# Kernel tuning notes

Measured on AMD Instinct MI355X. Metric: run time of the kernel, lower is better.

Reference implementation:

```python
import jax, jax.numpy as jnp
import numpy as np
from jax import lax

VOCAB = 32000
EMB = 1024
HID = 1024
SEQ = 128
BATCH = 32
FORGET_BIAS = 1.0


def setup_inputs() -> dict:
    key = jax.random.key(0)
    ks = jax.random.split(key, 8)
    u = lambda k, shape: jax.random.uniform(k, shape, jnp.float32, -0.1, 0.1)
    inp = {
        'input_seq': jax.random.randint(ks[0], (SEQ, BATCH), 0, VOCAB, dtype=jnp.int64),
        'emb': u(ks[1], (VOCAB, EMB)),
        # BasicLSTMCell kernel: [(input_dim + hidden), 4*hidden], bias [4*hidden]
        'W0': u(ks[2], (EMB + HID, 4 * HID)),
        'b0': jnp.zeros((4 * HID,), jnp.float32),
        'W1': u(ks[3], (HID + HID, 4 * HID)),
        'b1': jnp.zeros((4 * HID,), jnp.float32),
        'Wd': u(ks[4], (HID, VOCAB)),
        'bd': jnp.zeros((VOCAB,), jnp.float32),
    }
    return inp


def _lstm_layer(x_seq, W, b):
    """Static unrolled BasicLSTMCell as a lax.scan. x_seq: [T, B, D]."""
    T, B, _ = x_seq.shape
    H = b.shape[0] // 4

    def step(carry, x):
        c, h = carry
        z = jnp.concatenate([x, h], axis=-1) @ W + b  # [B, 4H]
        i, j, f, o = jnp.split(z, 4, axis=-1)  # gate order of BasicLSTMCell
        c2 = c * jax.nn.sigmoid(f + FORGET_BIAS) + jax.nn.sigmoid(i) * jnp.tanh(j)
        h2 = jnp.tanh(c2) * jax.nn.sigmoid(o)
        return (c2, h2), h2

    init = (jnp.zeros((B, H), x_seq.dtype), jnp.zeros((B, H), x_seq.dtype))
    _, ys = lax.scan(step, init, x_seq)
    return ys  # [T, B, H]


def reference(input_seq, emb, W0, b0, W1, b1, Wd, bd):
    y = emb[input_seq]                      # [T, B, EMB] embedding lookup
    y = _lstm_layer(y, W0, b0)              # layer 1
    y = _lstm_layer(y, W1, b1)              # layer 2
    logits = y.reshape(-1, y.shape[-1]) @ Wd + bd  # [T*B, VOCAB]
    return logits
```

## Files before the change

kernel.cpp:

```cpp
#include <hip/hip_runtime.h>

#define VOCAB 32000
#define EMB   1024
#define HID   1024
#define SEQ   128
#define BATCH 32
#define ROWS  (SEQ * BATCH)
#define G4    (4 * HID)
#define SSEG  512
#define SSLOT 65536

typedef __bf16 bf16x8 __attribute__((ext_vector_type(8)));
typedef float  f32x4  __attribute__((ext_vector_type(4)));

__device__ __forceinline__ unsigned short f2bf(float f) {
  union { float f; unsigned int u; } v; v.f = f;
  unsigned int r = v.u + 0x7fffu + ((v.u >> 16) & 1u);
  return (unsigned short)(r >> 16);
}
__device__ __forceinline__ float bf2f(unsigned short u) {
  union { unsigned int u; float f; } v; v.u = ((unsigned int)u) << 16;
  return v.f;
}

__device__ __forceinline__ void async16(const void* g, void* l) {
  __builtin_amdgcn_global_load_lds(
      (const __attribute__((address_space(1))) void*)g,
      (__attribute__((address_space(3))) void*)l, 16, 0, 0);
}

__device__ __forceinline__ float fsigmoid(float x) {
  return __builtin_amdgcn_rcpf(1.f + __expf(-x));
}
__device__ __forceinline__ float ftanh(float x) {
  return 1.f - 2.f * __builtin_amdgcn_rcpf(__expf(2.f * x) + 1.f);
}

__global__ void embed_split(const int* __restrict__ ids, const float* __restrict__ emb,
                            unsigned short* __restrict__ Xp) {
  int r = blockIdx.x;
  int t = r >> 5, b = r & 31;
  int row = ids[r];
  int e = threadIdx.x * 4;
  const float4 v = *reinterpret_cast<const float4*>(emb + (size_t)row * EMB + e);
  ushort4 hi, lo;
  hi.x = f2bf(v.x); lo.x = f2bf(v.x - bf2f(hi.x));
  hi.y = f2bf(v.y); lo.y = f2bf(v.y - bf2f(hi.y));
  hi.z = f2bf(v.z); lo.z = f2bf(v.z - bf2f(hi.z));
  hi.w = f2bf(v.w); lo.w = f2bf(v.w - bf2f(hi.w));
  unsigned short* dst = Xp + (size_t)t * SSLOT + (e >> 3) * SSEG + b * 16 + (e & 7);
  *reinterpret_cast<ushort4*>(dst)     = hi;
  *reinterpret_cast<ushort4*>(dst + 8) = lo;
}

__global__ void wsplit_kernel(const float* __restrict__ in, unsigned short* __restrict__ hi,
                              unsigned short* __restrict__ lo, int K, int N) {
  __shared__ float t[32][33];
  int n0 = blockIdx.x * 32, k0 = blockIdx.y * 32;
  int tx = threadIdx.x, ty = threadIdx.y;
#pragma unroll
  for (int i = 0; i < 4; ++i)
    t[ty + i * 8][tx] = in[(size_t)(k0 + ty + i * 8) * N + n0 + tx];
  __syncthreads();
#pragma unroll
  for (int i = 0; i < 4; ++i) {
    float v = t[tx][ty + i * 8];
    unsigned short h = f2bf(v);
    hi[(size_t)(n0 + ty + i * 8) * K + k0 + tx] = h;
    lo[(size_t)(n0 + ty + i * 8) * K + k0 + tx] = f2bf(v - bf2f(h));
  }
}

__global__ void transpose_kernel(const float* __restrict__ in, unsigned short* __restrict__ out,
                                 int K, int N) {
  __shared__ float t[32][33];
  int n0 = blockIdx.x * 32, k0 = blockIdx.y * 32;
  int tx = threadIdx.x, ty = threadIdx.y;
#pragma unroll
  for (int i = 0; i < 4; ++i)
    t[ty + i * 8][tx] = in[(size_t)(k0 + ty + i * 8) * N + n0 + tx];
  __syncthreads();
#pragma unroll
  for (int i = 0; i < 4; ++i)
    out[(size_t)(n0 + ty + i * 8) * K + k0 + tx] = f2bf(t[tx][ty + i * 8]);
}

__global__ __launch_bounds__(512, 2) void lstm_ring(
    const unsigned short* __restrict__ Xp,
    const unsigned short* __restrict__ W0hi, const unsigned short* __restrict__ W0lo,
    const unsigned short* __restrict__ W1hi, const unsigned short* __restrict__ W1lo,
    const float* __restrict__ b0, const float* __restrict__ b1,
    unsigned short* __restrict__ H2,
    unsigned short* h1r, unsigned short* h2r,
    unsigned int* F0, unsigned int* F1)
{
  __shared__ float zl[8][32][36];

  const int tid   = threadIdx.x;
  const int lane  = tid & 63;
  const int w     = tid >> 6;
  const int layer = blockIdx.x >> 7;
  const int wg    = blockIdx.x & 127;
  const int j0    = wg * 8;
  const int lrow  = lane & 15;
  const int klo   = (lane >> 4) * 8;

  const unsigned short* Whi = layer ? W1hi : W0hi;
  const unsigned short* Wlo = layer ? W1lo : W0lo;
  const float*          bias = layer ? b1 : b0;

  bf16x8 wh[2][8], wl[2][8];
#pragma unroll
  for (int nt = 0; nt < 2; ++nt) {
    int n = nt * 16 + lrow;
    size_t grow = (size_t)((n >> 3) * 1024 + j0 + (n & 7));
    const unsigned short* bh = Whi + grow * 2048 + w * 256 + klo;
    const unsigned short* bl = Wlo + grow * 2048 + w * 256 + klo;
#pragma unroll
    for (int ks = 0; ks < 8; ++ks) {
      wh[nt][ks] = *reinterpret_cast<const bf16x8*>(bh + ks * 32);
      wl[nt][ks] = *reinterpret_cast<const bf16x8*>(bl + ks * 32);
    }
  }

  const int eb = tid >> 3;
  const int ec = tid & 7;
  const float bi  = bias[j0 + ec];
  const float bj  = bias[1024 + j0 + ec];
  const float bff = bias[2048 + j0 + ec];
  const float bo  = bias[3072 + j0 + ec];
  float c = 0.f;

  unsigned int* Fown = layer ? F1 : F0;

  for (int t = 0; t < SEQ; ++t) {
    {
      const unsigned int* FF = nullptr;
      unsigned tgt = 0; int fb = 0;
      if (layer == 0) {
        if (w >= 4) { FF = F0; tgt = (unsigned)t; fb = (w - 4) * 32; }
      } else {
        if (w < 4) { FF = F0; tgt = (unsigned)(t + 1); fb = w * 32; }
        else       { FF = F1; tgt = (unsigned)t;       fb = (w - 4) * 32; }
      }
      if (FF && tgt) {
        for (;;) {
          unsigned v = (lane < 32)
              ? __hip_atomic_load(FF + (fb + lane) * 4, __ATOMIC_RELAXED,
                                  __HIP_MEMORY_SCOPE_AGENT)
              : 0xFFFFFFFFu;
          if (__all(v >= tgt)) break;
          __builtin_amdgcn_s_sleep(1);
        }
      }
      __builtin_amdgcn_sched_barrier(0);
    }

    const unsigned short* pb; int segb;
    if (layer == 0) {
      if (w < 4) { pb = Xp  + (size_t)t * SSLOT;       segb = w * 32; }
      else       { pb = h1r + (size_t)t * SSLOT;       segb = (w - 4) * 32; }
    } else {
      if (w < 4) { pb = h1r + (size_t)(t + 1) * SSLOT; segb = w * 32; }
      else       { pb = h2r + (size_t)t * SSLOT;       segb = (w - 4) * 32; }
    }
    const unsigned short* lanebase = pb + (size_t)(segb + (lane >> 4)) * SSEG + lrow * 16;

    f32x4 acc[2][2] = {};
#pragma unroll
    for (int ks = 0; ks < 8; ++ks) {
      const unsigned short* p = lanebase + ks * (4 * SSEG);
      bf16x8 a0h = *reinterpret_cast<const bf16x8*>(p);
      bf16x8 a0l = *reinterpret_cast<const bf16x8*>(p + 8);
      bf16x8 a1h = *reinterpret_cast<const bf16x8*>(p + 256);
      bf16x8 a1l = *reinterpret_cast<const bf16x8*>(p + 264);
#pragma unroll
      for (int nt = 0; nt < 2; ++nt) {
        acc[0][nt] = __builtin_amdgcn_mfma_f32_16x16x32_bf16(a0h, wh[nt][ks], acc[0][nt], 0, 0, 0);
        acc[0][nt] = __builtin_amdgcn_mfma_f32_16x16x32_bf16(a0l, wh[nt][ks], acc[0][nt], 0, 0, 0);
        acc[0][nt] = __builtin_amdgcn_mfma_f32_16x16x32_bf16(a0h, wl[nt][ks], acc[0][nt], 0, 0, 0);
        acc[1][nt] = __builtin_amdgcn_mfma_f32_16x16x32_bf16(a1h, wh[nt][ks], acc[1][nt], 0, 0, 0);
        acc[1][nt] = __builtin_amdgcn_mfma_f32_16x16x32_bf16(a1l, wh[nt][ks], acc[1][nt], 0, 0, 0);
        acc[1][nt] = __builtin_amdgcn_mfma_f32_16x16x32_bf16(a1h, wl[nt][ks], acc[1][nt], 0, 0, 0);
      }
    }

    const int zb = (lane >> 4) * 4;
#pragma unroll
    for (int mt = 0; mt < 2; ++mt)
#pragma unroll
      for (int nt = 0; nt < 2; ++nt)
#pragma unroll
        for (int j = 0; j < 4; ++j)
          zl[w][mt * 16 + zb + j][nt * 16 + lrow] = acc[mt][nt][j];
    __syncthreads();

    unsigned short hh = 0;
    if (tid < 256) {
      float iv = bi, jv = bj, fv = bff, ov = bo;
#pragma unroll
      for (int ww = 0; ww < 8; ++ww) {
        iv += zl[ww][eb][ec];
        jv += zl[ww][eb][8 + ec];
        fv += zl[ww][eb][16 + ec];
        ov += zl[ww][eb][24 + ec];
      }
      float si = fsigmoid(iv);
      float sf = fsigmoid(fv + 1.f);
      float so = fsigmoid(ov);
      float tj = ftanh(jv);
      c = c * sf + si * tj;
      float hv = ftanh(c) * so;
      hh = f2bf(hv);
      unsigned short hl = f2bf(hv - bf2f(hh));
      int hhp = __shfl_xor((int)hh, 1);
      int hlp = __shfl_xor((int)hl, 1);
      if ((ec & 1) == 0) {
        unsigned uhi = (unsigned)hh | ((unsigned)hhp << 16);
        unsigned ulo = (unsigned)hl | ((unsigned)hlp << 16);
        unsigned int* du = (unsigned int*)((layer ? h2r : h1r)
                           + (size_t)(t + 1) * SSLOT + wg * SSEG);
        unsigned uoff = (unsigned)(eb * 8 + (ec >> 1));
        __hip_atomic_store(du + uoff,     uhi, __ATOMIC_RELAXED, __HIP_MEMORY_SCOPE_AGENT);
        __hip_atomic_store(du + uoff + 4, ulo, __ATOMIC_RELAXED, __HIP_MEMORY_SCOPE_AGENT);
      }
    }
    __syncthreads();
    if (tid == 0)
      __hip_atomic_store(&Fown[wg * 4], (unsigned)(t + 1),
                         __ATOMIC_RELAXED, __HIP_MEMORY_SCOPE_AGENT);
    if (layer && tid < 256)
      H2[(size_t)(t * 32 + eb) * 1024 + j0 + ec] = hh;
  }
}

__global__ __launch_bounds__(256) void gemm_bt(
    const unsigned short* __restrict__ A, const unsigned short* __restrict__ B,
    const float* __restrict__ bias, float* __restrict__ C, int M, int N, int K)
{
  __shared__ __align__(16) unsigned short As[128 * 32];
  __shared__ __align__(16) unsigned short Bs[128 * 32];
  const int tid = threadIdx.x, lane = tid & 63, w = tid >> 6;

  const int ntiles = gridDim.x;
  int lid = blockIdx.y * ntiles + blockIdx.x;
  int total = ntiles * gridDim.y;
  int cpx = total >> 3;
  int swz = (lid & 7) * cpx + (lid >> 3);
  int bn = swz % ntiles, bm = swz / ntiles;

  const int wm = (w >> 1) * 64, wn = (w & 1) * 64;
  const int lrow = lane & 15, klo = (lane >> 4) * 8;
  const int l4 = lane >> 2, l2 = lane & 3;

  f32x4 acc[4][4] = {};

  for (int kt = 0; kt < K / 32; ++kt) {
    __syncthreads();
#pragma unroll
    for (int ci = 0; ci < 2; ++ci) {
      int row = w * 32 + ci * 16 + l4;
      async16(A + (size_t)(bm * 128 + row) * K + kt * 32 + l2 * 8,
              (char*)As + (w * 2 + ci) * 1024);
      async16(B + (size_t)(bn * 128 + row) * K + kt * 32 + l2 * 8,
              (char*)Bs + (w * 2 + ci) * 1024);
    }
    __syncthreads();
    bf16x8 a[4], bb[4];
#pragma unroll
    for (int i = 0; i < 4; ++i) {
      a[i]  = *reinterpret_cast<const bf16x8*>(As + (wm + i * 16 + lrow) * 32 + klo);
      bb[i] = *reinterpret_cast<const bf16x8*>(Bs + (wn + i * 16 + lrow) * 32 + klo);
    }
#pragma unroll
    for (int i = 0; i < 4; ++i)
#pragma unroll
      for (int j = 0; j < 4; ++j)
        acc[i][j] = __builtin_amdgcn_mfma_f32_16x16x32_bf16(a[i], bb[j], acc[i][j], 0, 0, 0);
  }

#pragma unroll
  for (int j2 = 0; j2 < 4; ++j2) {
    int col = bn * 128 + wn + j2 * 16 + lrow;
    float bv = bias[col];
#pragma unroll
    for (int i = 0; i < 4; ++i) {
      int rbase = bm * 128 + wm + i * 16 + (lane >> 4) * 4;
#pragma unroll
      for (int j = 0; j < 4; ++j)
        C[(size_t)(rbase + j) * N + col] = acc[i][j2][j] + bv;
    }
  }
}

extern "C" void kernel_launch(void* const* d_in, const int* in_sizes, int n_in,
                              void* d_out, int out_size, void* d_ws, size_t ws_size,
                              hipStream_t stream) {
  const int*   ids = (const int*)d_in[0];
  const float* emb = (const float*)d_in[1];
  const float* W0  = (const float*)d_in[2];
  const float* b0  = (const float*)d_in[3];
  const float* W1  = (const float*)d_in[4];
  const float* b1  = (const float*)d_in[5];
  const float* Wd  = (const float*)d_in[6];
  const float* bd  = (const float*)d_in[7];
  float* out = (float*)d_out;

  unsigned short* Xp  = (unsigned short*)d_out;
  unsigned short* h1r = Xp + (size_t)SEQ * SSLOT;
  unsigned short* h2r = h1r + (size_t)(SEQ + 1) * SSLOT;

  char* ws = (char*)d_ws;
  size_t off = 0;
  auto alloc = [&](size_t bytes) {
    char* p = ws + off;
    off += (bytes + 255) & ~(size_t)255;
    return p;
  };
  unsigned int*   F0 = (unsigned int*)alloc(2048);
  unsigned int*   F1 = (unsigned int*)alloc(2048);
  unsigned short* H2 = (unsigned short*)alloc((size_t)ROWS * HID * 2);
  size_t regionW = off;
  unsigned short* W0hi = (unsigned short*)alloc((size_t)G4 * 2048 * 2);
  unsigned short* W0lo = (unsigned short*)alloc((size_t)G4 * 2048 * 2);
  unsigned short* W1hi = (unsigned short*)alloc((size_t)G4 * 2048 * 2);
  unsigned short* W1lo = (unsigned short*)alloc((size_t)G4 * 2048 * 2);
  unsigned short* Wdt  = (unsigned short*)(ws + regionW);
  (void)in_sizes; (void)n_in; (void)out_size; (void)ws_size;

  hipMemsetAsync(F0, 0, 4096, stream);
  hipMemsetAsync(h1r, 0, (size_t)SSLOT * 2, stream);
  hipMemsetAsync(h2r, 0, (size_t)SSLOT * 2, stream);

  embed_split<<<ROWS, 256, 0, stream>>>(ids, emb, Xp);
  wsplit_kernel<<<dim3(G4 / 32, 2048 / 32), dim3(32, 8), 0, stream>>>(W0, W0hi, W0lo, 2048, G4);
  wsplit_kernel<<<dim3(G4 / 32, 2048 / 32), dim3(32, 8), 0, stream>>>(W1, W1hi, W1lo, 2048, G4);

  lstm_ring<<<256, 512, 0, stream>>>(Xp, W0hi, W0lo, W1hi, W1lo, b0, b1,
                                     H2, h1r, h2r, F0, F1);

  transpose_kernel<<<dim3(VOCAB / 32, HID / 32), dim3(32, 8), 0, stream>>>(Wd, Wdt, HID, VOCAB);
  gemm_bt<<<dim3(VOCAB / 128, ROWS / 128), 256, 0, stream>>>(H2, Wdt, bd, out,
                                                             ROWS, VOCAB, HID);
}
```

Measured before the change: 1.237 ms.

## Fuse LSTM weight split into persistent kernel and swizzle GEMM LDS layout

Removes the two wsplit pre-pass kernels: the persistent LSTM kernel now reads the raw fp32 weights directly and splits them into bf16 hi/lo register fragments at startup. This drops a full write and re-read of the split weight buffers. The load pattern is strided, one column element per row, so it is uncoalesced, but it runs once per block. The output GEMM gains an XOR swizzle on LDS tile placement and reads, to reduce bank conflicts. The Wd transpose is moved ahead of the LSTM and given its own workspace buffer.

```diff
diff --git a/kernel.cpp b/kernel.cpp
--- a/kernel.cpp
+++ b/kernel.cpp
@@ -53,24 +53,6 @@
   *reinterpret_cast<ushort4*>(dst + 8) = lo;
 }
 
-__global__ void wsplit_kernel(const float* __restrict__ in, unsigned short* __restrict__ hi,
-                              unsigned short* __restrict__ lo, int K, int N) {
-  __shared__ float t[32][33];
-  int n0 = blockIdx.x * 32, k0 = blockIdx.y * 32;
-  int tx = threadIdx.x, ty = threadIdx.y;
-#pragma unroll
-  for (int i = 0; i < 4; ++i)
-    t[ty + i * 8][tx] = in[(size_t)(k0 + ty + i * 8) * N + n0 + tx];
-  __syncthreads();
-#pragma unroll
-  for (int i = 0; i < 4; ++i) {
-    float v = t[tx][ty + i * 8];
-    unsigned short h = f2bf(v);
-    hi[(size_t)(n0 + ty + i * 8) * K + k0 + tx] = h;
-    lo[(size_t)(n0 + ty + i * 8) * K + k0 + tx] = f2bf(v - bf2f(h));
-  }
-}
-
 __global__ void transpose_kernel(const float* __restrict__ in, unsigned short* __restrict__ out,
                                  int K, int N) {
   __shared__ float t[32][33];
@@ -87,8 +69,7 @@
 
 __global__ __launch_bounds__(512, 2) void lstm_ring(
     const unsigned short* __restrict__ Xp,
-    const unsigned short* __restrict__ W0hi, const unsigned short* __restrict__ W0lo,
-    const unsigned short* __restrict__ W1hi, const unsigned short* __restrict__ W1lo,
+    const float* __restrict__ W0, const float* __restrict__ W1,
     const float* __restrict__ b0, const float* __restrict__ b1,
     unsigned short* __restrict__ H2,
     unsigned short* h1r, unsigned short* h2r,
@@ -105,21 +86,25 @@
   const int lrow  = lane & 15;
   const int klo   = (lane >> 4) * 8;
 
-  const unsigned short* Whi = layer ? W1hi : W0hi;
-  const unsigned short* Wlo = layer ? W1lo : W0lo;
-  const float*          bias = layer ? b1 : b0;
+  const float* Wraw = layer ? W1 : W0;
+  const float* bias = layer ? b1 : b0;
 
   bf16x8 wh[2][8], wl[2][8];
 #pragma unroll
   for (int nt = 0; nt < 2; ++nt) {
-    int n = nt * 16 + lrow;
-    size_t grow = (size_t)((n >> 3) * 1024 + j0 + (n & 7));
-    const unsigned short* bh = Whi + grow * 2048 + w * 256 + klo;
-    const unsigned short* bl = Wlo + grow * 2048 + w * 256 + klo;
+    int n   = nt * 16 + lrow;
+    int col = (n >> 3) * 1024 + j0 + (n & 7);
 #pragma unroll
     for (int ks = 0; ks < 8; ++ks) {
-      wh[nt][ks] = *reinterpret_cast<const bf16x8*>(bh + ks * 32);
-      wl[nt][ks] = *reinterpret_cast<const bf16x8*>(bl + ks * 32);
+      alignas(16) unsigned short th[8], tl[8];
+#pragma unroll
+      for (int e = 0; e < 8; ++e) {
+        float v = Wraw[(size_t)(w * 256 + ks * 32 + klo + e) * G4 + col];
+        th[e] = f2bf(v);
+        tl[e] = f2bf(v - bf2f(th[e]));
+      }
+      wh[nt][ks] = *reinterpret_cast<bf16x8*>(th);
+      wl[nt][ks] = *reinterpret_cast<bf16x8*>(tl);
     }
   }
 
@@ -250,7 +235,7 @@
   int bn = swz % ntiles, bm = swz / ntiles;
 
   const int wm = (w >> 1) * 64, wn = (w & 1) * 64;
-  const int lrow = lane & 15, klo = (lane >> 4) * 8;
+  const int lrow = lane & 15;
   const int l4 = lane >> 2, l2 = lane & 3;
 
   f32x4 acc[4][4] = {};
@@ -260,17 +245,20 @@
 #pragma unroll
     for (int ci = 0; ci < 2; ++ci) {
       int row = w * 32 + ci * 16 + l4;
-      async16(A + (size_t)(bm * 128 + row) * K + kt * 32 + l2 * 8,
+      int sw  = l2 ^ ((row >> 1) & 3);
+      async16(A + (size_t)(bm * 128 + row) * K + kt * 32 + sw * 8,
               (char*)As + (w * 2 + ci) * 1024);
-      async16(B + (size_t)(bn * 128 + row) * K + kt * 32 + l2 * 8,
+      async16(B + (size_t)(bn * 128 + row) * K + kt * 32 + sw * 8,
               (char*)Bs + (w * 2 + ci) * 1024);
     }
     __syncthreads();
     bf16x8 a[4], bb[4];
 #pragma unroll
     for (int i = 0; i < 4; ++i) {
-      a[i]  = *reinterpret_cast<const bf16x8*>(As + (wm + i * 16 + lrow) * 32 + klo);
-      bb[i] = *reinterpret_cast<const bf16x8*>(Bs + (wn + i * 16 + lrow) * 32 + klo);
+      int ra = wm + i * 16 + lrow;
+      int rb = wn + i * 16 + lrow;
+      a[i]  = *reinterpret_cast<const bf16x8*>(As + ra * 32 + (((lane >> 4) ^ ((ra >> 1) & 3)) * 8));
+      bb[i] = *reinterpret_cast<const bf16x8*>(Bs + rb * 32 + (((lane >> 4) ^ ((rb >> 1) & 3)) * 8));
     }
 #pragma unroll
     for (int i = 0; i < 4; ++i)
@@ -317,15 +305,10 @@
     off += (bytes + 255) & ~(size_t)255;
     return p;
   };
-  unsigned int*   F0 = (unsigned int*)alloc(2048);
-  unsigned int*   F1 = (unsigned int*)alloc(2048);
-  unsigned short* H2 = (unsigned short*)alloc((size_t)ROWS * HID * 2);
-  size_t regionW = off;
-  unsigned short* W0hi = (unsigned short*)alloc((size_t)G4 * 2048 * 2);
-  unsigned short* W0lo = (unsigned short*)alloc((size_t)G4 * 2048 * 2);
-  unsigned short* W1hi = (unsigned short*)alloc((size_t)G4 * 2048 * 2);
-  unsigned short* W1lo = (unsigned short*)alloc((size_t)G4 * 2048 * 2);
-  unsigned short* Wdt  = (unsigned short*)(ws + regionW);
+  unsigned int*   F0  = (unsigned int*)alloc(2048);
+  unsigned int*   F1  = (unsigned int*)alloc(2048);
+  unsigned short* H2  = (unsigned short*)alloc((size_t)ROWS * HID * 2);
+  unsigned short* Wdt = (unsigned short*)alloc((size_t)VOCAB * HID * 2);
   (void)in_sizes; (void)n_in; (void)out_size; (void)ws_size;
 
   hipMemsetAsync(F0, 0, 4096, stream);
@@ -333,13 +316,10 @@
   hipMemsetAsync(h2r, 0, (size_t)SSLOT * 2, stream);
 
   embed_split<<<ROWS, 256, 0, stream>>>(ids, emb, Xp);
-  wsplit_kernel<<<dim3(G4 / 32, 2048 / 32), dim3(32, 8), 0, stream>>>(W0, W0hi, W0lo, 2048, G4);
-  wsplit_kernel<<<dim3(G4 / 32, 2048 / 32), dim3(32, 8), 0, stream>>>(W1, W1hi, W1lo, 2048, G4);
-
-  lstm_ring<<<256, 512, 0, stream>>>(Xp, W0hi, W0lo, W1hi, W1lo, b0, b1,
-                                     H2, h1r, h2r, F0, F1);
-
   transpose_kernel<<<dim3(VOCAB / 32, HID / 32), dim3(32, 8), 0, stream>>>(Wd, Wdt, HID, VOCAB);
+
+  lstm_ring<<<256, 512, 0, stream>>>(Xp, W0, W1, b0, b1, H2, h1r, h2r, F0, F1);
+
   gemm_bt<<<dim3(VOCAB / 128, ROWS / 128), 256, 0, stream>>>(H2, Wdt, bd, out,
                                                              ROWS, VOCAB, HID);
 }
```

New measurement: 1.217 ms. No clear change (-1.7%).
